# Kernel optimization log

Hardware: AMD Instinct MI355X
Metric: run time of the kernel (lower is better)

## Reference

```python
import jax, jax.numpy as jnp
import numpy as np

N, E, C, NTT, NMOL = 200000, 1600000, 128, 20000, 2000
EPS = 1e-5


def setup_inputs() -> dict:
    key = jax.random.key(0)
    ks = jax.random.split(key, 32)
    s = 0.05
    d = {}
    d["node_attr"] = jax.random.normal(ks[0], (N, C), jnp.float32)
    d["adj_index"] = jax.random.randint(ks[1], (2, E), 0, N)
    d["adj_value"] = jax.random.uniform(ks[2], (E,), jnp.float32)
    d["tt_node_batch"] = jnp.sort(jax.random.randint(ks[3], (N,), 0, NTT))
    d["tt_graph_batch"] = jnp.sort(jax.random.randint(ks[4], (NTT,), 0, NMOL))
    # GCN layers (2): linear weight/bias
    d["W_gcn"] = jax.random.normal(ks[5], (2, C, C)) * s
    d["b_gcn"] = jnp.zeros((2, C))
    # 8 BatchNorm1d(C): [gcn0, gcn1, tt0, tt1, tt2, mol0, mol1, mol2] (eval mode)
    d["bn_gamma"] = jnp.ones((8, C))
    d["bn_beta"] = jnp.zeros((8, C))
    d["bn_mean"] = jnp.zeros((8, C))
    d["bn_var"] = jnp.ones((8, C))
    # 2 GATConv (tt, mol): bipartite lin_src/lin_dst, att_src/att_dst, bias (heads=1)
    d["gat_Wsrc"] = jax.random.normal(ks[6], (2, C, C)) * s
    d["gat_Wdst"] = jax.random.normal(ks[7], (2, C, C)) * s
    d["gat_asrc"] = jax.random.normal(ks[8], (2, C)) * s
    d["gat_adst"] = jax.random.normal(ks[9], (2, C)) * s
    d["gat_bias"] = jnp.zeros((2, C))
    # 2 GRUCell(C, C)
    d["gru_Wih"] = jax.random.normal(ks[10], (2, 3 * C, C)) * s
    d["gru_Whh"] = jax.random.normal(ks[11], (2, 3 * C, C)) * s
    d["gru_bih"] = jnp.zeros((2, 3 * C))
    d["gru_bhh"] = jnp.zeros((2, 3 * C))
    # predictor: 128 -> 64 (relu) -> 1
    d["pW1"] = jax.random.normal(ks[12], (64, C)) * s
    d["pb1"] = jnp.full((64,), 0.01)
    d["pW2"] = jax.random.normal(ks[13], (1, 64)) * s
    d["pb2"] = jnp.full((1,), 0.01)
    return d


def _bn(x, i, g, b, m, v):
    return (x - m[i]) * (g[i] / jnp.sqrt(v[i] + EPS)) + b[i]


def _spmm(idx, val, x, n):  # out[i] = sum_j A[i,j] x[j]
    return jax.ops.segment_sum(val[:, None] * x[idx[1]], idx[0], num_segments=n)


def _gat(x_src, x_dst, src, dst, nseg, Ws, Wd, a_s, a_d, bias):
    hs = x_src @ Ws.T
    hd = x_dst @ Wd.T
    alpha = jax.nn.leaky_relu(hs @ a_s, 0.01 * 0 + 0.01) if False else None
    a = (hs @ a_s)[src] + (hd @ a_d)[dst]
    a = jnp.where(a > 0, a, 0.01 * a)  # leaky_relu, negative_slope=0.01
    mx = jax.ops.segment_max(a, dst, num_segments=nseg)
    e = jnp.exp(a - mx[dst])
    den = jax.ops.segment_sum(e, dst, num_segments=nseg)
    w = e / den[dst]
    return jax.ops.segment_sum(w[:, None] * hs[src], dst, num_segments=nseg) + bias


def _gru(x, h, Wih, Whh, bih, bhh):
    gi = x @ Wih.T + bih
    gh = h @ Whh.T + bhh
    ir, iz, inn = jnp.split(gi, 3, axis=-1)
    hr, hz, hn = jnp.split(gh, 3, axis=-1)
    r = jax.nn.sigmoid(ir + hr)
    z = jax.nn.sigmoid(iz + hz)
    n = jnp.tanh(inn + r * hn)
    return (1.0 - z) * n + z * h


def _pool_stage(x, seg, nseg, bn_base, gi, bn_gamma, bn_beta, bn_mean, bn_var,
                gat_Wsrc, gat_Wdst, gat_asrc, gat_adst, gat_bias,
                gru_Wih, gru_Whh, gru_bih, gru_bhh):
    x = _bn(x, bn_base, bn_gamma, bn_beta, bn_mean, bn_var)
    mean = jax.ops.segment_sum(x, seg, num_segments=nseg)  # global_add_pool
    mean = _bn(jax.nn.relu(mean), bn_base + 1, bn_gamma, bn_beta, bn_mean, bn_var)
    src = jnp.arange(x.shape[0])
    g = _gat(x, mean, src, seg, nseg, gat_Wsrc[gi], gat_Wdst[gi], gat_asrc[gi], gat_adst[gi], gat_bias[gi])
    g = jax.nn.elu(g)  # dropout p=0.001 is identity in eval
    g = _gru(g, mean, gru_Wih[gi], gru_Whh[gi], gru_bih[gi], gru_bhh[gi])
    return _bn(jax.nn.relu(g), bn_base + 2, bn_gamma, bn_beta, bn_mean, bn_var)


def reference(node_attr, adj_value, W_gcn, b_gcn, bn_gamma, bn_beta, bn_mean, bn_var,
              gat_Wsrc, gat_Wdst, gat_asrc, gat_adst, gat_bias,
              gru_Wih, gru_Whh, gru_bih, gru_bhh, pW1, pb1, pW2, pb2,
              adj_index, tt_node_batch, tt_graph_batch):
    # graph embedder: two GCN layers  x <- relu(BN(A @ (x W^T) + b))
    x = node_attr
    for i in range(2):
        x = _spmm(adj_index, adj_value, x @ W_gcn[i].T, N) + b_gcn[i]
        x = jax.nn.relu(_bn(x, i, bn_gamma, bn_beta, bn_mean, bn_var))
    # tt pooling: nodes -> tt subgraphs
    tt = _pool_stage(x, tt_node_batch, NTT, 2, 0, bn_gamma, bn_beta, bn_mean, bn_var,
                     gat_Wsrc, gat_Wdst, gat_asrc, gat_adst, gat_bias,
                     gru_Wih, gru_Whh, gru_bih, gru_bhh)
    # mol pooling: tt subgraphs -> molecules
    mol = _pool_stage(tt, tt_graph_batch, NMOL, 5, 1, bn_gamma, bn_beta, bn_mean, bn_var,
                      gat_Wsrc, gat_Wdst, gat_asrc, gat_adst, gat_bias,
                      gru_Wih, gru_Whh, gru_bih, gru_bhh)
    # predictor
    h = jax.nn.relu(mol @ pW1.T + pb1)
    return h @ pW2.T + pb2  # [NMOL, 1]
```

## Files before the change

kernel.cpp:

```cpp
#include <hip/hip_runtime.h>
#include <math.h>

#define CCH 128
#define G3  384
#define BN_EPS 1e-5f
#define BSH 9
#define BROWS 512
#define COLBITS 19

typedef __bf16 bf16;
typedef __bf16 bf16x2 __attribute__((ext_vector_type(2)));
typedef __bf16 bf16x4 __attribute__((ext_vector_type(4)));
typedef __bf16 bf16x8 __attribute__((ext_vector_type(8)));
typedef float f32x4 __attribute__((ext_vector_type(4)));

__global__ __launch_bounds__(256) void prep_kernel(
    const float* __restrict__ g, const float* __restrict__ b,
    const float* __restrict__ m, const float* __restrict__ v,
    float* __restrict__ bnsc, float* __restrict__ bnsh,
    const float* __restrict__ Wsrc, const float* __restrict__ Wdst,
    const float* __restrict__ asrc, const float* __restrict__ adst,
    float* __restrict__ vsp, float* __restrict__ vd, float* __restrict__ c0,
    const int* __restrict__ tt_node_batch, int N, int NTT, int* __restrict__ starts_tt,
    const int* __restrict__ tt_graph_batch, int NMOL, int* __restrict__ starts_mol,
    int* __restrict__ bhist,
    const float* __restrict__ Wgcn, bf16* __restrict__ Wgcnb,
    bf16* __restrict__ Wsrcb,
    const float* __restrict__ Wih, bf16* __restrict__ Wihb,
    const float* __restrict__ Whh, bf16* __restrict__ Whhb,
    int B1, int B2, int B3, int B4, int B5, int B6, int B7, int B8)
{
    __shared__ float red[2];
    const int bid = blockIdx.x;
    const int tid = threadIdx.x;
    if (bid < B1) {
        int idx = bid * 256 + tid;
        if (idx < 8 * CCH) {
            float s = g[idx] / sqrtf(v[idx] + BN_EPS);
            bnsc[idx] = s;
            bnsh[idx] = b[idx] - m[idx] * s;
        }
    } else if (bid < B2) {
        int s = bid - B1;
        int which = tid >> 7, k = tid & 127;
        const float* W = (which ? Wdst : Wsrc) + s * CCH * CCH;
        const float* a = (which ? adst : asrc) + s * CCH;
        float acc = 0.f;
        for (int j = 0; j < CCH; ++j) acc += W[j * CCH + k] * a[j];
        if (which) {
            vd[s * CCH + k] = acc;
        } else {
            int l = 2 + 3 * s;
            float scl = g[l * CCH + k] / sqrtf(v[l * CCH + k] + BN_EPS);
            float shf = b[l * CCH + k] - m[l * CCH + k] * scl;
            vsp[s * CCH + k] = acc * scl;
            float p = shf * acc;
            for (int o = 32; o; o >>= 1) p += __shfl_down(p, o);
            if ((k & 63) == 0) red[k >> 6] = p;
        }
        __syncthreads();
        if (tid == 0) c0[s] = red[0] + red[1];
    } else if (bid < B3) {
        int s = (bid - B2) * 256 + tid;
        if (s <= NTT) {
            int lo = 0, hi = N;
            while (lo < hi) { int mid = (lo + hi) >> 1; if (tt_node_batch[mid] < s) lo = mid + 1; else hi = mid; }
            starts_tt[s] = lo;
        }
    } else if (bid < B4) {
        int s = (bid - B3) * 256 + tid;
        if (s <= NMOL) {
            int lo = 0, hi = NTT;
            while (lo < hi) { int mid = (lo + hi) >> 1; if (tt_graph_batch[mid] < s) lo = mid + 1; else hi = mid; }
            starts_mol[s] = lo;
        }
    } else if (bid < B5) {
        bhist[tid] = 0; bhist[tid + 256] = 0;
    } else {
        const float* src; bf16* dst; int i0, n4;
        if (bid < B6)      { src = Wgcn; dst = Wgcnb; i0 = (bid - B5) * 256; n4 = 2 * CCH * CCH / 4; }
        else if (bid < B7) { src = Wsrc; dst = Wsrcb; i0 = (bid - B6) * 256; n4 = 2 * CCH * CCH / 4; }
        else if (bid < B8) { src = Wih;  dst = Wihb;  i0 = (bid - B7) * 256; n4 = 2 * G3 * CCH / 4; }
        else               { src = Whh;  dst = Whhb;  i0 = (bid - B8) * 256; n4 = 2 * G3 * CCH / 4; }
        int i = i0 + tid;
        if (i < n4) {
            float4 x = ((const float4*)src)[i];
            bf16x4 o = { (bf16)x.x, (bf16)x.y, (bf16)x.z, (bf16)x.w };
            ((bf16x4*)dst)[i] = o;
        }
    }
}


__global__ __launch_bounds__(256) void bucket_hist_kernel(const int* __restrict__ rows,
                                                          int* __restrict__ bhist, int E)
{
    __shared__ int h[512];
    int t = threadIdx.x;
    h[t] = 0; h[t + 256] = 0;
    __syncthreads();
    int base = blockIdx.x * 4096;
#pragma unroll
    for (int i = 0; i < 16; ++i) {
        int e = base + i * 256 + t;
        if (e < E) atomicAdd(&h[rows[e] >> BSH], 1);
    }
    __syncthreads();
    if (h[t]) atomicAdd(&bhist[t], h[t]);
    if (h[t + 256]) atomicAdd(&bhist[t + 256], h[t + 256]);
}

__global__ __launch_bounds__(256) void bucket_scan_kernel(const int* __restrict__ bhist,
                                                          int* __restrict__ boff, int* __restrict__ bcur,
                                                          int* __restrict__ row_ptr, int NB, int N, int E)
{
    __shared__ int h[512], sx[512], wt[4];
    int t = threadIdx.x;
    h[t] = bhist[t]; h[t + 256] = bhist[t + 256];
    __syncthreads();
    int v0 = h[2 * t], v1 = h[2 * t + 1];
    int s = v0 + v1, incl = s;
    for (int o = 1; o < 64; o <<= 1) { int u = __shfl_up(incl, o); if ((t & 63) >= o) incl += u; }
    if ((t & 63) == 63) wt[t >> 6] = incl;
    __syncthreads();
    int woff = 0, w = t >> 6;
    for (int i = 0; i < w; ++i) woff += wt[i];
    int excl = woff + incl - s;
    sx[2 * t] = excl; sx[2 * t + 1] = excl + v0;
    __syncthreads();
    if (t < NB)       { boff[t] = sx[t];       bcur[t] = sx[t]; }
    if (t + 256 < NB) { boff[t + 256] = sx[t + 256]; bcur[t + 256] = sx[t + 256]; }
    if (t == 0) { boff[NB] = E; row_ptr[N] = E; }
}

__global__ __launch_bounds__(256) void bucket_bin_kernel(
    const int* __restrict__ rows, const int* __restrict__ cols, const float* __restrict__ val,
    int* __restrict__ bcur, int2* __restrict__ bcv, int E)
{
    __shared__ int hist[512], sx[512], cnt[512], gbase[512], wt[4];
    __shared__ int mb[4096];
    __shared__ int2 mcv[4096];
    int t = threadIdx.x;
    hist[t] = 0; hist[t + 256] = 0; cnt[t] = 0; cnt[t + 256] = 0;
    __syncthreads();
    int base = blockIdx.x * 4096;
    int r[16];
#pragma unroll
    for (int i = 0; i < 16; ++i) {
        int e = base + i * 256 + t;
        r[i] = (e < E) ? rows[e] : -1;
        if (r[i] >= 0) atomicAdd(&hist[r[i] >> BSH], 1);
    }
    __syncthreads();
    int v0 = hist[2 * t], v1 = hist[2 * t + 1];
    int s = v0 + v1, incl = s;
    for (int o = 1; o < 64; o <<= 1) { int u = __shfl_up(incl, o); if ((t & 63) >= o) incl += u; }
    if ((t & 63) == 63) wt[t >> 6] = incl;
    __syncthreads();
    int woff = 0, w = t >> 6;
    for (int i = 0; i < w; ++i) woff += wt[i];
    int excl = woff + incl - s;
    sx[2 * t] = excl; sx[2 * t + 1] = excl + v0;
    __syncthreads();
    for (int bb = t; bb < 512; bb += 256)
        if (hist[bb]) gbase[bb] = atomicAdd(&bcur[bb], hist[bb]);
    __syncthreads();
#pragma unroll
    for (int i = 0; i < 16; ++i) {
        if (r[i] < 0) continue;
        int e = base + i * 256 + t;
        int bb = r[i] >> BSH;
        int p = atomicAdd(&cnt[bb], 1);
        int loc = sx[bb] + p;
        mb[loc] = bb;
        int2 cv;
        cv.x = cols[e] | ((r[i] & (BROWS - 1)) << COLBITS);
        cv.y = __float_as_int(val[e]);
        mcv[loc] = cv;
    }
    __syncthreads();
    int Mv = sx[511] + hist[511];
    for (int loc = t; loc < Mv; loc += 256) {
        int bb = mb[loc];
        int gidx = gbase[bb] + (loc - sx[bb]);
        bcv[gidx] = mcv[loc];
    }
}

__global__ __launch_bounds__(256) void bucket_place_kernel(
    const int2* __restrict__ bcv, const int* __restrict__ boff, int* __restrict__ row_ptr,
    int2* __restrict__ cpack, int N)
{
    __shared__ int rcnt[512], sx[512], wt[4];
    int b = blockIdx.x;
    int t = threadIdx.x;
    rcnt[t] = 0; rcnt[t + 256] = 0;
    __syncthreads();
    int rbase = b << BSH;
    int rn = min(BROWS, N - rbase);
    int lo = boff[b], hi = boff[b + 1];
    for (int p = lo + t; p < hi; p += 256)
        atomicAdd(&rcnt[((unsigned)bcv[p].x) >> COLBITS], 1);
    __syncthreads();
    int v0 = rcnt[2 * t], v1 = rcnt[2 * t + 1];
    int s = v0 + v1, incl = s;
    for (int o = 1; o < 64; o <<= 1) { int u = __shfl_up(incl, o); if ((t & 63) >= o) incl += u; }
    if ((t & 63) == 63) wt[t >> 6] = incl;
    __syncthreads();
    int woff = 0, w = t >> 6;
    for (int i = 0; i < w; ++i) woff += wt[i];
    int excl = woff + incl - s;
    sx[2 * t] = excl; sx[2 * t + 1] = excl + v0;
    __syncthreads();
    if (t < rn)       row_ptr[rbase + t] = lo + sx[t];
    if (t + 256 < rn) row_ptr[rbase + t + 256] = lo + sx[t + 256];
    __syncthreads();
    sx[t] += lo; sx[t + 256] += lo;
    __syncthreads();
    for (int p = lo + t; p < hi; p += 256) {
        int2 cv = bcv[p];
        int rin = ((unsigned)cv.x) >> COLBITS;
        int slot = atomicAdd(&sx[rin], 1);
        cv.x &= (1 << COLBITS) - 1;
        cpack[slot] = cv;
    }
}

template<int IN_BF16, int OUT_BF16, int ACT>
__global__ __launch_bounds__(256, 2) void gemm_mfma(
    const void* __restrict__ Xv, const bf16* __restrict__ W,
    const float* __restrict__ bias, void* __restrict__ Yv, int M, int Nout)
{
    __shared__ bf16 Xs[128 * 136];
    __shared__ bf16 Ws[128 * 136];
    const int tid = threadIdx.x;
    const int rb = blockIdx.x * 128;
    const int cb = blockIdx.y * 128;

#pragma unroll
    for (int i = 0; i < 8; ++i) {
        int c = tid + i * 256;
        int r = c >> 4, k8 = (c & 15) << 3;
        *(bf16x8*)&Ws[r * 136 + k8] = *(const bf16x8*)&W[(size_t)(cb + r) * CCH + k8];
    }
    if (IN_BF16) {
#pragma unroll
        for (int i = 0; i < 8; ++i) {
            int c = tid + i * 256;
            int r = c >> 4, k8 = (c & 15) << 3;
            int grow = rb + r;
            bf16x8 o = {};
            if (grow < M) o = *(const bf16x8*)&((const bf16*)Xv)[(size_t)grow * CCH + k8];
            *(bf16x8*)&Xs[r * 136 + k8] = o;
        }
    } else {
#pragma unroll
        for (int i = 0; i < 16; ++i) {
            int c = tid + i * 256;
            int r = c >> 5, k4 = (c & 31) << 2;
            int grow = rb + r;
            bf16x4 o = {};
            if (grow < M) {
                float4 xv = *(const float4*)&((const float*)Xv)[(size_t)grow * CCH + k4];
                o[0] = (bf16)xv.x; o[1] = (bf16)xv.y; o[2] = (bf16)xv.z; o[3] = (bf16)xv.w;
            }
            *(bf16x4*)&Xs[r * 136 + k4] = o;
        }
    }
    __syncthreads();

    const int w = tid >> 6, lane = tid & 63;
    const int col16 = lane & 15, quad = lane >> 4;
    const int wm = (w & 1) * 64, wn = (w >> 1) * 64;

    f32x4 acc[4][4] = {};
#pragma unroll
    for (int kk = 0; kk < 4; ++kk) {
        bf16x8 af[4], bfr[4];
#pragma unroll
        for (int mi = 0; mi < 4; ++mi)
            af[mi] = *(const bf16x8*)&Xs[(wm + mi * 16 + col16) * 136 + kk * 32 + quad * 8];
#pragma unroll
        for (int ni = 0; ni < 4; ++ni)
            bfr[ni] = *(const bf16x8*)&Ws[(wn + ni * 16 + col16) * 136 + kk * 32 + quad * 8];
#pragma unroll
        for (int mi = 0; mi < 4; ++mi)
#pragma unroll
            for (int ni = 0; ni < 4; ++ni)
                acc[mi][ni] = __builtin_amdgcn_mfma_f32_16x16x32_bf16(af[mi], bfr[ni], acc[mi][ni], 0, 0, 0);
    }

#pragma unroll
    for (int mi = 0; mi < 4; ++mi) {
#pragma unroll
        for (int r = 0; r < 4; ++r) {
            int row = rb + wm + mi * 16 + quad * 4 + r;
            if (row >= M) continue;
#pragma unroll
            for (int ni = 0; ni < 4; ++ni) {
                int col = cb + wn + ni * 16 + col16;
                float vv = acc[mi][ni][r];
                if (bias) vv += bias[col];
                if (ACT == 1) vv = vv > 0.f ? vv : expm1f(vv);
                if (OUT_BF16) ((bf16*)Yv)[(size_t)row * Nout + col] = (bf16)vv;
                else          ((float*)Yv)[(size_t)row * Nout + col] = vv;
            }
        }
    }
}

__global__ __launch_bounds__(256, 2) void gemm_dual(
    const float* __restrict__ X0, const bf16* __restrict__ W0,
    const float* __restrict__ b0, float* __restrict__ Y0,
    const float* __restrict__ X1, const bf16* __restrict__ W1,
    const float* __restrict__ b1, float* __restrict__ Y1, int M)
{
    __shared__ bf16 Xs[128 * 136];
    __shared__ bf16 Ws[128 * 136];
    const int tid = threadIdx.x;
    const int rb = blockIdx.x * 128;
    const int yy = blockIdx.y;
    const float* X; const bf16* W; const float* bias; float* Y; int cb;
    if (yy < 3) { X = X0; W = W0; bias = b0; Y = Y0; cb = yy * 128; }
    else        { X = X1; W = W1; bias = b1; Y = Y1; cb = (yy - 3) * 128; }

#pragma unroll
    for (int i = 0; i < 8; ++i) {
        int c = tid + i * 256;
        int r = c >> 4, k8 = (c & 15) << 3;
        *(bf16x8*)&Ws[r * 136 + k8] = *(const bf16x8*)&W[(size_t)(cb + r) * CCH + k8];
    }
#pragma unroll
    for (int i = 0; i < 16; ++i) {
        int c = tid + i * 256;
        int r = c >> 5, k4 = (c & 31) << 2;
        int grow = rb + r;
        bf16x4 o = {};
        if (grow < M) {
            float4 xv = *(const float4*)&X[(size_t)grow * CCH + k4];
            o[0] = (bf16)xv.x; o[1] = (bf16)xv.y; o[2] = (bf16)xv.z; o[3] = (bf16)xv.w;
        }
        *(bf16x4*)&Xs[r * 136 + k4] = o;
    }
    __syncthreads();

    const int w = tid >> 6, lane = tid & 63;
    const int col16 = lane & 15, quad = lane >> 4;
    const int wm = (w & 1) * 64, wn = (w >> 1) * 64;

    f32x4 acc[4][4] = {};
#pragma unroll
    for (int kk = 0; kk < 4; ++kk) {
        bf16x8 af[4], bfr[4];
#pragma unroll
        for (int mi = 0; mi < 4; ++mi)
            af[mi] = *(const bf16x8*)&Xs[(wm + mi * 16 + col16) * 136 + kk * 32 + quad * 8];
#pragma unroll
        for (int ni = 0; ni < 4; ++ni)
            bfr[ni] = *(const bf16x8*)&Ws[(wn + ni * 16 + col16) * 136 + kk * 32 + quad * 8];
#pragma unroll
        for (int mi = 0; mi < 4; ++mi)
#pragma unroll
            for (int ni = 0; ni < 4; ++ni)
                acc[mi][ni] = __builtin_amdgcn_mfma_f32_16x16x32_bf16(af[mi], bfr[ni], acc[mi][ni], 0, 0, 0);
    }

#pragma unroll
    for (int mi = 0; mi < 4; ++mi) {
#pragma unroll
        for (int r = 0; r < 4; ++r) {
            int row = rb + wm + mi * 16 + quad * 4 + r;
            if (row >= M) continue;
#pragma unroll
            for (int ni = 0; ni < 4; ++ni) {
                int col = cb + wn + ni * 16 + col16;
                Y[(size_t)row * G3 + col] = acc[mi][ni][r] + bias[col];
            }
        }
    }
}

template<int SCORES>
__global__ __launch_bounds__(256) void spmm_csr_kernel(
    const int* __restrict__ row_ptr, const int2* __restrict__ cpack,
    const bf16* __restrict__ Xin, bf16* __restrict__ Y,
    const float* __restrict__ bvec, const float* __restrict__ sc, const float* __restrict__ sh,
    const float* __restrict__ vsp, const float* __restrict__ c0p, float* __restrict__ scores,
    int Nrow)
{
    int gid = blockIdx.x * 256 + threadIdx.x;
    int row = gid >> 4;
    if (row >= Nrow) return;
    int l8 = (gid & 15) << 3;
    int st = row_ptr[row], en = row_ptr[row + 1];
    float acc[8] = {};
    int j = st;
    for (; j + 4 <= en; j += 4) {
        int2 p0 = cpack[j], p1 = cpack[j + 1], p2 = cpack[j + 2], p3 = cpack[j + 3];
        bf16x8 x0 = *(const bf16x8*)&Xin[(size_t)p0.x * CCH + l8];
        bf16x8 x1 = *(const bf16x8*)&Xin[(size_t)p1.x * CCH + l8];
        bf16x8 x2 = *(const bf16x8*)&Xin[(size_t)p2.x * CCH + l8];
        bf16x8 x3 = *(const bf16x8*)&Xin[(size_t)p3.x * CCH + l8];
        float v0 = __int_as_float(p0.y), v1 = __int_as_float(p1.y);
        float v2 = __int_as_float(p2.y), v3 = __int_as_float(p3.y);
#pragma unroll
        for (int q = 0; q < 8; ++q)
            acc[q] += v0 * (float)x0[q] + v1 * (float)x1[q] + v2 * (float)x2[q] + v3 * (float)x3[q];
    }
    if (j + 2 <= en) {
        int2 p0 = cpack[j], p1 = cpack[j + 1];
        bf16x8 x0 = *(const bf16x8*)&Xin[(size_t)p0.x * CCH + l8];
        bf16x8 x1 = *(const bf16x8*)&Xin[(size_t)p1.x * CCH + l8];
        float v0 = __int_as_float(p0.y), v1 = __int_as_float(p1.y);
#pragma unroll
        for (int q = 0; q < 8; ++q) acc[q] += v0 * (float)x0[q] + v1 * (float)x1[q];
        j += 2;
    }
    if (j < en) {
        int2 p0 = cpack[j];
        bf16x8 x0 = *(const bf16x8*)&Xin[(size_t)p0.x * CCH + l8];
        float v0 = __int_as_float(p0.y);
#pragma unroll
        for (int q = 0; q < 8; ++q) acc[q] += v0 * (float)x0[q];
    }
    float o[8];
    bf16x8 ov;
#pragma unroll
    for (int q = 0; q < 8; ++q) {
        o[q] = fmaxf((acc[q] + bvec[l8 + q]) * sc[l8 + q] + sh[l8 + q], 0.f);
        ov[q] = (bf16)o[q];
    }
    *(bf16x8*)&Y[(size_t)row * CCH + l8] = ov;
    if (SCORES) {
        float p = 0.f;
#pragma unroll
        for (int q = 0; q < 8; ++q) p += o[q] * vsp[l8 + q];
        for (int d = 8; d; d >>= 1) p += __shfl_down(p, d, 16);
        if ((gid & 15) == 0) scores[row] = p + c0p[0];
    }
}

__global__ __launch_bounds__(128) void segstage_kernel(
    const bf16* __restrict__ X, const float* __restrict__ sarr, const int* __restrict__ starts,
    const float* __restrict__ sc2, const float* __restrict__ sh2,
    const float* __restrict__ sc3, const float* __restrict__ sh3,
    const float* __restrict__ vd, float* __restrict__ mean, float* __restrict__ upool)
{
    __shared__ float red[2];
    __shared__ float adsh;
    int t = blockIdx.x;
    int c = threadIdx.x;
    int st = starts[t], en = starts[t + 1];
    float sum = 0.f;
    for (int i = st; i < en; ++i) sum += (float)X[(size_t)i * CCH + c];
    float cnt = (float)(en - st);
    float poolb = fmaxf(sum * sc2[c] + cnt * sh2[c], 0.f);
    float mv = poolb * sc3[c] + sh3[c];
    mean[(size_t)t * CCH + c] = mv;
    float p = mv * vd[c];
    for (int o = 32; o; o >>= 1) p += __shfl_down(p, o);
    if ((c & 63) == 0) red[c >> 6] = p;
    __syncthreads();
    if (c == 0) adsh = red[0] + red[1];
    __syncthreads();
    if (en == st) { upool[(size_t)t * CCH + c] = 0.f; return; }
    float adt = adsh;
    float lm = -3.0e38f;
    for (int i = st + c; i < en; i += 128) {
        float a = sarr[i] + adt;
        a = a > 0.f ? a : 0.01f * a;
        lm = fmaxf(lm, a);
    }
    for (int o = 32; o; o >>= 1) lm = fmaxf(lm, __shfl_down(lm, o));
    if ((c & 63) == 0) red[c >> 6] = lm;
    __syncthreads();
    float m = fmaxf(red[0], red[1]);
    float u = 0.f, den = 0.f;
    for (int i = st; i < en; ++i) {
        float a = sarr[i] + adt;
        a = a > 0.f ? a : 0.01f * a;
        float e = __expf(a - m);
        den += e;
        u += e * (float)X[(size_t)i * CCH + c];
    }
    upool[(size_t)t * CCH + c] = (u / den) * sc2[c] + sh2[c];
}

__global__ __launch_bounds__(256) void gru_kernel(
    const float* __restrict__ giM, const float* __restrict__ ghM, const float* __restrict__ mean,
    const float* __restrict__ sc4, const float* __restrict__ sh4,
    bf16* __restrict__ out,
    const float* __restrict__ vsp2, const float* __restrict__ c02, float* __restrict__ scores,
    int total)
{
    __shared__ float sred[4];
    int idx = blockIdx.x * 256 + threadIdx.x;
    bool ok = idx < total;
    int t = idx >> 7, c = idx & 127;
    float o = 0.f;
    if (ok) {
        size_t b = (size_t)t * G3;
        float ir = giM[b + c],  iz = giM[b + 128 + c], inn = giM[b + 256 + c];
        float hr = ghM[b + c],  hz = ghM[b + 128 + c], hn  = ghM[b + 256 + c];
        float r = 1.f / (1.f + __expf(-(ir + hr)));
        float z = 1.f / (1.f + __expf(-(iz + hz)));
        float nn = tanhf(inn + r * hn);
        float h = (1.f - z) * nn + z * mean[idx];
        h = fmaxf(h, 0.f);
        o = h * sc4[c] + sh4[c];
        out[idx] = (bf16)o;
    }
    float p = ok ? o * vsp2[c] : 0.f;
    for (int d = 32; d; d >>= 1) p += __shfl_down(p, d);
    int w = threadIdx.x >> 6;
    if ((threadIdx.x & 63) == 0) sred[w] = p;
    __syncthreads();
    if (threadIdx.x == 0 && ok)   scores[t] = sred[0] + sred[1] + c02[0];
    if (threadIdx.x == 128 && ok) scores[t] = sred[2] + sred[3] + c02[0];
}

__global__ __launch_bounds__(256) void gru_pred_kernel(
    const float* __restrict__ giM, const float* __restrict__ ghM, const float* __restrict__ mean,
    const float* __restrict__ sc4, const float* __restrict__ sh4,
    const float* __restrict__ pW1, const float* __restrict__ pb1,
    const float* __restrict__ pW2, const float* __restrict__ pb2,
    float* __restrict__ out, int nseg)
{
    __shared__ float row[2][CCH];
    int half = threadIdx.x >> 7;
    int c = threadIdx.x & 127;
    int t = blockIdx.x * 2 + half;
    bool ok = t < nseg;
    float o = 0.f;
    if (ok) {
        size_t b = (size_t)t * G3;
        float ir = giM[b + c],  iz = giM[b + 128 + c], inn = giM[b + 256 + c];
        float hr = ghM[b + c],  hz = ghM[b + 128 + c], hn  = ghM[b + 256 + c];
        float r = 1.f / (1.f + __expf(-(ir + hr)));
        float z = 1.f / (1.f + __expf(-(iz + hz)));
        float nn = tanhf(inn + r * hn);
        float h = (1.f - z) * nn + z * mean[(size_t)t * CCH + c];
        h = fmaxf(h, 0.f);
        o = h * sc4[c] + sh4[c];
    }
    row[half][c] = o;
    __syncthreads();
    if (c < 64 && ok) {
        float h = pb1[c];
#pragma unroll
        for (int k = 0; k < CCH; ++k) h += row[half][k] * pW1[c * CCH + k];
        h = fmaxf(h, 0.f);
        float p = h * pW2[c];
        for (int d = 32; d; d >>= 1) p += __shfl_down(p, d);
        if (c == 0) out[t] = p + pb2[0];
    }
}


extern "C" void kernel_launch(void* const* d_in, const int* in_sizes, int n_in,
                              void* d_out, int out_size, void* d_ws, size_t ws_size,
                              hipStream_t stream)
{
    (void)n_in; (void)ws_size;
    const float* node_attr      = (const float*)d_in[0];
    const int*   adj_index      = (const int*)  d_in[1];
    const float* adj_value      = (const float*)d_in[2];
    const int*   tt_node_batch  = (const int*)  d_in[3];
    const int*   tt_graph_batch = (const int*)  d_in[4];
    const float* W_gcn    = (const float*)d_in[5];
    const float* b_gcn    = (const float*)d_in[6];
    const float* bn_gamma = (const float*)d_in[7];
    const float* bn_beta  = (const float*)d_in[8];
    const float* bn_mean  = (const float*)d_in[9];
    const float* bn_var   = (const float*)d_in[10];
    const float* gat_Wsrc = (const float*)d_in[11];
    const float* gat_Wdst = (const float*)d_in[12];
    const float* gat_asrc = (const float*)d_in[13];
    const float* gat_adst = (const float*)d_in[14];
    const float* gat_bias = (const float*)d_in[15];
    const float* gru_Wih  = (const float*)d_in[16];
    const float* gru_Whh  = (const float*)d_in[17];
    const float* gru_bih  = (const float*)d_in[18];
    const float* gru_bhh  = (const float*)d_in[19];
    const float* pW1 = (const float*)d_in[20];
    const float* pb1 = (const float*)d_in[21];
    const float* pW2 = (const float*)d_in[22];
    const float* pb2 = (const float*)d_in[23];

    const int E    = in_sizes[2];
    const int N    = in_sizes[3];
    const int NTT  = in_sizes[4];
    const int NMOL = out_size;
    const int NB   = (N + BROWS - 1) >> BSH;

    const int* adj_rows = adj_index;
    const int* adj_cols = adj_index + E;

    char* wsb = (char*)d_ws;
    size_t off = 0;
    auto carve = [&](size_t bytes) -> char* {
        char* p = wsb + off;
        off = (off + bytes + 255) & ~(size_t)255;
        return p;
    };
    bf16* bufB = (bf16*)carve((size_t)N * CCH * 2);
    bf16* bufA = (bf16*)carve((size_t)N * CCH * 2);
    bf16* tt   = (bf16*)carve((size_t)NTT * CCH * 2);
    float* mean  = (float*)carve((size_t)NTT * CCH * 4);
    float* upool = (float*)carve((size_t)NTT * CCH * 4);
    float* gbuf  = (float*)carve((size_t)NTT * CCH * 4);
    float* giM   = (float*)carve((size_t)NTT * G3 * 4);
    float* ghM   = (float*)carve((size_t)NTT * G3 * 4);
    float* scores = (float*)carve((size_t)N * 4);
    int* starts_tt  = (int*)carve((size_t)(NTT + 1) * 4);
    int* starts_mol = (int*)carve((size_t)(NMOL + 1) * 4);
    float* bnsc = (float*)carve(8 * CCH * 4);
    float* bnsh = (float*)carve(8 * CCH * 4);
    float* vsp  = (float*)carve(2 * CCH * 4);
    float* vd   = (float*)carve(2 * CCH * 4);
    float* c0   = (float*)carve(2 * 4);
    bf16* Wgcnb = (bf16*)carve((size_t)2 * CCH * CCH * 2);
    bf16* Wsrcb = (bf16*)carve((size_t)2 * CCH * CCH * 2);
    bf16* Wihb  = (bf16*)carve((size_t)2 * G3 * CCH * 2);
    bf16* Whhb  = (bf16*)carve((size_t)2 * G3 * CCH * 2);
    int*   bhist   = (int*)carve(512 * 4);
    int*   boff    = (int*)carve((size_t)(NB + 1) * 4);
    int*   bcur    = (int*)carve((size_t)NB * 4);
    int*   row_ptr = (int*)carve((size_t)(N + 1) * 4);
    int2*  bcv     = (int2*)carve((size_t)E * 8);
    int2*  cpack   = (int2*)carve((size_t)E * 8);

    const int B1 = 4;
    const int B2 = B1 + 2;
    const int B3 = B2 + (NTT + 1 + 255) / 256;
    const int B4 = B3 + (NMOL + 1 + 255) / 256;
    const int B5 = B4 + 1;
    const int B6 = B5 + 32;
    const int B7 = B6 + 32;
    const int B8 = B7 + 96;
    const int B9 = B8 + 96;
    prep_kernel<<<B9, 256, 0, stream>>>(
        bn_gamma, bn_beta, bn_mean, bn_var, bnsc, bnsh,
        gat_Wsrc, gat_Wdst, gat_asrc, gat_adst, vsp, vd, c0,
        tt_node_batch, N, NTT, starts_tt,
        tt_graph_batch, NMOL, starts_mol,
        bhist,
        W_gcn, Wgcnb, Wsrcb, gru_Wih, Wihb, gru_Whh, Whhb,
        B1, B2, B3, B4, B5, B6, B7, B8);

    const int nchunk = (E + 4095) / 4096;
    bucket_hist_kernel<<<nchunk, 256, 0, stream>>>(adj_rows, bhist, E);
    bucket_scan_kernel<<<1, 256, 0, stream>>>(bhist, boff, bcur, row_ptr, NB, N, E);
    bucket_bin_kernel<<<nchunk, 256, 0, stream>>>(adj_rows, adj_cols, adj_value, bcur, bcv, E);
    bucket_place_kernel<<<NB, 256, 0, stream>>>(bcv, boff, row_ptr, cpack, N);

    dim3 gg((N + 127) / 128, 1);
    const int spmm_blocks = ((size_t)N * 16 + 255) / 256;
    gemm_mfma<0, 1, 0><<<gg, 256, 0, stream>>>(node_attr, Wgcnb, nullptr, bufB, N, CCH);
    spmm_csr_kernel<0><<<spmm_blocks, 256, 0, stream>>>(
        row_ptr, cpack, bufB, bufA, b_gcn, bnsc, bnsh, nullptr, nullptr, nullptr, N);
    gemm_mfma<1, 1, 0><<<gg, 256, 0, stream>>>(bufA, Wgcnb + CCH * CCH, nullptr, bufB, N, CCH);
    spmm_csr_kernel<1><<<spmm_blocks, 256, 0, stream>>>(
        row_ptr, cpack, bufB, bufA, b_gcn + CCH, bnsc + CCH, bnsh + CCH,
        vsp, c0, scores, N);

    {
        const int bnb = 2, gi = 0, nseg = NTT;
        segstage_kernel<<<nseg, 128, 0, stream>>>(bufA, scores, starts_tt,
            bnsc + bnb * CCH, bnsh + bnb * CCH, bnsc + (bnb + 1) * CCH, bnsh + (bnb + 1) * CCH,
            vd + gi * CCH, mean, upool);
        dim3 g1((nseg + 127) / 128, 1);
        gemm_mfma<0, 0, 1><<<g1, 256, 0, stream>>>(upool, Wsrcb + gi * CCH * CCH,
                                                   gat_bias + gi * CCH, gbuf, nseg, CCH);
        dim3 g2((nseg + 127) / 128, 6);
        gemm_dual<<<g2, 256, 0, stream>>>(gbuf, Wihb + gi * G3 * CCH, gru_bih + gi * G3, giM,
                                          mean, Whhb + gi * G3 * CCH, gru_bhh + gi * G3, ghM, nseg);
        gru_kernel<<<(nseg * CCH + 255) / 256, 256, 0, stream>>>(giM, ghM, mean,
            bnsc + (bnb + 2) * CCH, bnsh + (bnb + 2) * CCH, tt,
            vsp + CCH, c0 + 1, scores, nseg * CCH);
    }

    {
        const int bnb = 5, gi = 1, nseg = NMOL;
        segstage_kernel<<<nseg, 128, 0, stream>>>(tt, scores, starts_mol,
            bnsc + bnb * CCH, bnsh + bnb * CCH, bnsc + (bnb + 1) * CCH, bnsh + (bnb + 1) * CCH,
            vd + gi * CCH, mean, upool);
        dim3 g1((nseg + 127) / 128, 1);
        gemm_mfma<0, 0, 1><<<g1, 256, 0, stream>>>(upool, Wsrcb + gi * CCH * CCH,
                                                   gat_bias + gi * CCH, gbuf, nseg, CCH);
        dim3 g2((nseg + 127) / 128, 6);
        gemm_dual<<<g2, 256, 0, stream>>>(gbuf, Wihb + gi * G3 * CCH, gru_bih + gi * G3, giM,
                                          mean, Whhb + gi * G3 * CCH, gru_bhh + gi * G3, ghM, nseg);
        gru_pred_kernel<<<(nseg + 1) / 2, 256, 0, stream>>>(giM, ghM, mean,
            bnsc + (bnb + 2) * CCH, bnsh + (bnb + 2) * CCH,
            pW1, pb1, pW2, pb2, (float*)d_out, nseg);
    }
}
```

Before: 612.4 us.

## Pre-swizzle bf16 weights into MFMA fragment layout and read directly from global

```diff
diff --git a/kernel.cpp b/kernel.cpp
--- a/kernel.cpp
+++ b/kernel.cpp
@@ -77,17 +77,20 @@
     } else if (bid < B5) {
         bhist[tid] = 0; bhist[tid + 256] = 0;
     } else {
-        const float* src; bf16* dst; int i0, n4;
-        if (bid < B6)      { src = Wgcn; dst = Wgcnb; i0 = (bid - B5) * 256; n4 = 2 * CCH * CCH / 4; }
-        else if (bid < B7) { src = Wsrc; dst = Wsrcb; i0 = (bid - B6) * 256; n4 = 2 * CCH * CCH / 4; }
-        else if (bid < B8) { src = Wih;  dst = Wihb;  i0 = (bid - B7) * 256; n4 = 2 * G3 * CCH / 4; }
-        else               { src = Whh;  dst = Whhb;  i0 = (bid - B8) * 256; n4 = 2 * G3 * CCH / 4; }
-        int i = i0 + tid;
-        if (i < n4) {
-            float4 x = ((const float4*)src)[i];
-            bf16x4 o = { (bf16)x.x, (bf16)x.y, (bf16)x.z, (bf16)x.w };
-            ((bf16x4*)dst)[i] = o;
-        }
+        const float* src; bf16* dst; int u0;
+        if (bid < B6)      { src = Wgcn; dst = Wgcnb; u0 = (bid - B5) * 256; }
+        else if (bid < B7) { src = Wsrc; dst = Wsrcb; u0 = (bid - B6) * 256; }
+        else if (bid < B8) { src = Wih;  dst = Wihb;  u0 = (bid - B7) * 256; }
+        else               { src = Whh;  dst = Whhb;  u0 = (bid - B8) * 256; }
+        int u = u0 + tid;
+        int row = u >> 4, kc = u & 15;
+        int bi = row >> 7, nrow = row & 127;
+        const float* s = src + (size_t)row * CCH + kc * 8;
+        float4 a = *(const float4*)s;
+        float4 b4 = *(const float4*)(s + 4);
+        bf16x8 o = { (bf16)a.x, (bf16)a.y, (bf16)a.z, (bf16)a.w,
+                     (bf16)b4.x, (bf16)b4.y, (bf16)b4.z, (bf16)b4.w };
+        *(bf16x8*)&dst[(size_t)bi * 16384 + ((kc * 128 + nrow) << 3)] = o;
     }
 }
 
@@ -226,45 +229,41 @@
     }
 }
 
+
 template<int IN_BF16, int OUT_BF16, int ACT>
-__global__ __launch_bounds__(256, 2) void gemm_mfma(
-    const void* __restrict__ Xv, const bf16* __restrict__ W,
+__global__ __launch_bounds__(256, 4) void gemm_mfma(
+    const void* __restrict__ Xv, const bf16* __restrict__ Wf,
     const float* __restrict__ bias, void* __restrict__ Yv, int M, int Nout)
 {
-    __shared__ bf16 Xs[128 * 136];
-    __shared__ bf16 Ws[128 * 136];
+    __shared__ bf16 Xs[128 * 128];
     const int tid = threadIdx.x;
     const int rb = blockIdx.x * 128;
     const int cb = blockIdx.y * 128;
-
-#pragma unroll
-    for (int i = 0; i < 8; ++i) {
-        int c = tid + i * 256;
-        int r = c >> 4, k8 = (c & 15) << 3;
-        *(bf16x8*)&Ws[r * 136 + k8] = *(const bf16x8*)&W[(size_t)(cb + r) * CCH + k8];
-    }
+    const bf16* Wfb = Wf + (size_t)cb * CCH;
+
     if (IN_BF16) {
 #pragma unroll
         for (int i = 0; i < 8; ++i) {
             int c = tid + i * 256;
-            int r = c >> 4, k8 = (c & 15) << 3;
+            int r = c >> 4, kc = c & 15;
             int grow = rb + r;
             bf16x8 o = {};
-            if (grow < M) o = *(const bf16x8*)&((const bf16*)Xv)[(size_t)grow * CCH + k8];
-            *(bf16x8*)&Xs[r * 136 + k8] = o;
+            if (grow < M) o = *(const bf16x8*)&((const bf16*)Xv)[(size_t)grow * CCH + kc * 8];
+            *(bf16x8*)&Xs[(r * 16 + (kc ^ (r & 15))) << 3] = o;
         }
     } else {
 #pragma unroll
         for (int i = 0; i < 16; ++i) {
             int c = tid + i * 256;
-            int r = c >> 5, k4 = (c & 31) << 2;
+            int r = c >> 5, sub = c & 31;
+            int kc = sub >> 1, half = sub & 1;
             int grow = rb + r;
             bf16x4 o = {};
             if (grow < M) {
-                float4 xv = *(const float4*)&((const float*)Xv)[(size_t)grow * CCH + k4];
+                float4 xv = *(const float4*)&((const float*)Xv)[(size_t)grow * CCH + kc * 8 + half * 4];
                 o[0] = (bf16)xv.x; o[1] = (bf16)xv.y; o[2] = (bf16)xv.z; o[3] = (bf16)xv.w;
             }
-            *(bf16x4*)&Xs[r * 136 + k4] = o;
+            *(bf16x4*)&Xs[((r * 16 + (kc ^ (r & 15))) << 3) + half * 4] = o;
         }
     }
     __syncthreads();
@@ -276,13 +275,16 @@
     f32x4 acc[4][4] = {};
 #pragma unroll
     for (int kk = 0; kk < 4; ++kk) {
-        bf16x8 af[4], bfr[4];
-#pragma unroll
-        for (int mi = 0; mi < 4; ++mi)
-            af[mi] = *(const bf16x8*)&Xs[(wm + mi * 16 + col16) * 136 + kk * 32 + quad * 8];
+        const int kc = kk * 4 + quad;
+        bf16x8 bfr[4], af[4];
 #pragma unroll
         for (int ni = 0; ni < 4; ++ni)
-            bfr[ni] = *(const bf16x8*)&Ws[(wn + ni * 16 + col16) * 136 + kk * 32 + quad * 8];
+            bfr[ni] = *(const bf16x8*)&Wfb[(size_t)((kc * 128 + wn + ni * 16 + col16) << 3)];
+#pragma unroll
+        for (int mi = 0; mi < 4; ++mi) {
+            int r = wm + mi * 16 + col16;
+            af[mi] = *(const bf16x8*)&Xs[(r * 16 + (kc ^ col16)) << 3];
+        }
 #pragma unroll
         for (int mi = 0; mi < 4; ++mi)
 #pragma unroll
@@ -309,38 +311,33 @@
     }
 }
 
-__global__ __launch_bounds__(256, 2) void gemm_dual(
+__global__ __launch_bounds__(256, 4) void gemm_dual(
     const float* __restrict__ X0, const bf16* __restrict__ W0,
     const float* __restrict__ b0, float* __restrict__ Y0,
     const float* __restrict__ X1, const bf16* __restrict__ W1,
     const float* __restrict__ b1, float* __restrict__ Y1, int M)
 {
-    __shared__ bf16 Xs[128 * 136];
-    __shared__ bf16 Ws[128 * 136];
+    __shared__ bf16 Xs[128 * 128];
     const int tid = threadIdx.x;
     const int rb = blockIdx.x * 128;
     const int yy = blockIdx.y;
     const float* X; const bf16* W; const float* bias; float* Y; int cb;
     if (yy < 3) { X = X0; W = W0; bias = b0; Y = Y0; cb = yy * 128; }
     else        { X = X1; W = W1; bias = b1; Y = Y1; cb = (yy - 3) * 128; }
-
-#pragma unroll
-    for (int i = 0; i < 8; ++i) {
-        int c = tid + i * 256;
-        int r = c >> 4, k8 = (c & 15) << 3;
-        *(bf16x8*)&Ws[r * 136 + k8] = *(const bf16x8*)&W[(size_t)(cb + r) * CCH + k8];
-    }
+    const bf16* Wfb = W + (size_t)cb * CCH;
+
 #pragma unroll
     for (int i = 0; i < 16; ++i) {
         int c = tid + i * 256;
-        int r = c >> 5, k4 = (c & 31) << 2;
+        int r = c >> 5, sub = c & 31;
+        int kc = sub >> 1, half = sub & 1;
         int grow = rb + r;
         bf16x4 o = {};
         if (grow < M) {
-            float4 xv = *(const float4*)&X[(size_t)grow * CCH + k4];
+            float4 xv = *(const float4*)&X[(size_t)grow * CCH + kc * 8 + half * 4];
             o[0] = (bf16)xv.x; o[1] = (bf16)xv.y; o[2] = (bf16)xv.z; o[3] = (bf16)xv.w;
         }
-        *(bf16x4*)&Xs[r * 136 + k4] = o;
+        *(bf16x4*)&Xs[((r * 16 + (kc ^ (r & 15))) << 3) + half * 4] = o;
     }
     __syncthreads();
 
@@ -351,13 +348,16 @@
     f32x4 acc[4][4] = {};
 #pragma unroll
     for (int kk = 0; kk < 4; ++kk) {
-        bf16x8 af[4], bfr[4];
-#pragma unroll
-        for (int mi = 0; mi < 4; ++mi)
-            af[mi] = *(const bf16x8*)&Xs[(wm + mi * 16 + col16) * 136 + kk * 32 + quad * 8];
+        const int kc = kk * 4 + quad;
+        bf16x8 bfr[4], af[4];
 #pragma unroll
         for (int ni = 0; ni < 4; ++ni)
-            bfr[ni] = *(const bf16x8*)&Ws[(wn + ni * 16 + col16) * 136 + kk * 32 + quad * 8];
+            bfr[ni] = *(const bf16x8*)&Wfb[(size_t)((kc * 128 + wn + ni * 16 + col16) << 3)];
+#pragma unroll
+        for (int mi = 0; mi < 4; ++mi) {
+            int r = wm + mi * 16 + col16;
+            af[mi] = *(const bf16x8*)&Xs[(r * 16 + (kc ^ col16)) << 3];
+        }
 #pragma unroll
         for (int mi = 0; mi < 4; ++mi)
 #pragma unroll
@@ -635,10 +635,10 @@
     const int B3 = B2 + (NTT + 1 + 255) / 256;
     const int B4 = B3 + (NMOL + 1 + 255) / 256;
     const int B5 = B4 + 1;
-    const int B6 = B5 + 32;
-    const int B7 = B6 + 32;
-    const int B8 = B7 + 96;
-    const int B9 = B8 + 96;
+    const int B6 = B5 + 16;
+    const int B7 = B6 + 16;
+    const int B8 = B7 + 48;
+    const int B9 = B8 + 48;
     prep_kernel<<<B9, 256, 0, stream>>>(
         bn_gamma, bn_beta, bn_mean, bn_var, bnsc, bnsh,
         gat_Wsrc, gat_Wdst, gat_asrc, gat_adst, vsp, vd, c0,
```

Measured after the change: 595.4 us. 1.03x faster.
